# Kernel tuning notes

Hardware: AMD Instinct MI355X
Metric: run time of the kernel (lower is better)

Reference implementation:

```python
import jax, jax.numpy as jnp
import numpy as np

WS = 7
C = 384
NH = 12
HD = C // NH
HID = 4 * C


def layernorm(x, g, b, eps=1e-5):
    m = jnp.mean(x, axis=-1, keepdims=True)
    v = jnp.mean((x - m) ** 2, axis=-1, keepdims=True)
    return (x - m) * jax.lax.rsqrt(v + eps) * g + b


def setup_inputs() -> dict:
    key = jax.random.key(0)
    ks = jax.random.split(key, 12)
    s = 0.02
    return {
        "tokens": jax.random.normal(ks[0], (2, 8, 56 * 56, C), jnp.float32),
        "in_proj_w": jax.random.normal(ks[1], (3 * C, C), jnp.float32) * s,
        "in_proj_b": jnp.zeros((3 * C,), jnp.float32),
        "out_w": jax.random.normal(ks[2], (C, C), jnp.float32) * s,
        "out_b": jnp.zeros((C,), jnp.float32),
        "ln1_g": jnp.ones((C,), jnp.float32),
        "ln1_b": jnp.zeros((C,), jnp.float32),
        "w1": jax.random.normal(ks[3], (HID, C), jnp.float32) * s,
        "b1": jnp.zeros((HID,), jnp.float32),
        "w2": jax.random.normal(ks[4], (C, HID), jnp.float32) * s,
        "b2": jnp.zeros((C,), jnp.float32),
        "ln2_g": jnp.ones((C,), jnp.float32),
        "ln2_b": jnp.zeros((C,), jnp.float32),
        "h": 56,
        "w": 56,
    }


def _block(tokens, in_proj_w, in_proj_b, out_w, out_b, ln1_g, ln1_b, w1, b1, w2, b2, ln2_g, ln2_b, h, w):
    b, t, _, c = tokens.shape
    orig_h, orig_w = h, w
    x = tokens.reshape(b, t, h, w, c)
    pad_h = (-h) % WS
    pad_w = (-w) % WS
    if pad_h > 0 or pad_w > 0:
        x = jnp.pad(x, ((0, 0), (0, 0), (0, pad_h), (0, pad_w), (0, 0)))
        h, w = h + pad_h, w + pad_w
    nh, nw = h // WS, w // WS
    # window partition -> [N, 49, C]
    x = x.reshape(b, t, nh, WS, nw, WS, c).transpose(0, 1, 2, 4, 3, 5, 6)
    win = x.reshape(b * t * nh * nw, WS * WS, c)
    # MHA (torch nn.MultiheadAttention semantics)
    a = layernorm(win, ln1_g, ln1_b)
    qkv = a @ in_proj_w.T + in_proj_b  # [N, 49, 3C]
    q, k, v = jnp.split(qkv, 3, axis=-1)
    n, s, _ = q.shape
    q = q.reshape(n, s, NH, HD).transpose(0, 2, 1, 3)
    k = k.reshape(n, s, NH, HD).transpose(0, 2, 1, 3)
    v = v.reshape(n, s, NH, HD).transpose(0, 2, 1, 3)
    scores = jnp.einsum("nhqd,nhkd->nhqk", q, k) / jnp.sqrt(jnp.asarray(HD, q.dtype))
    p = jax.nn.softmax(scores, axis=-1)
    o = jnp.einsum("nhqk,nhkd->nhqd", p, v).transpose(0, 2, 1, 3).reshape(n, s, c)
    win = win + (o @ out_w.T + out_b)
    # MLP
    m = layernorm(win, ln2_g, ln2_b)
    m = jax.nn.gelu(m @ w1.T + b1, approximate=False) @ w2.T + b2
    win = win + m
    # window reverse
    x = win.reshape(b, t, nh, nw, WS, WS, c).transpose(0, 1, 2, 4, 3, 5, 6).reshape(b, t, h, w, c)
    x = x[:, :, :orig_h, :orig_w, :]
    return x.reshape(b, t, orig_h * orig_w, c)


def reference(tokens, in_proj_w, in_proj_b, out_w, out_b, ln1_g, ln1_b, w1, b1, w2, b2, ln2_g, ln2_b, h, w):
    return _block(tokens, in_proj_w, in_proj_b, out_w, out_b, ln1_g, ln1_b, w1, b1, w2, b2, ln2_g, ln2_b, h, w)
```

## Files before the change

### kernel.cpp

```cpp
#include <hip/hip_runtime.h>
#include <hip/hip_bf16.h>
#include <math.h>

using short8 = __attribute__((ext_vector_type(8))) short;
using f32x4  = __attribute__((ext_vector_type(4))) float;

#define MFMA_B16(A,B,C) __builtin_amdgcn_mfma_f32_16x16x32_bf16((A),(B),(C),0,0,0)

#define ALN_STR 392
#define ALN_SZ  38416
#define POOL    76832
#define PS      34816
#define Q2_OFF  0
#define K2_OFF  7056
#define VT_OFF  14112
#define OH_OFF  23328
#define HIDB    17408
#define QK_STR  72
#define VT_STR  72
#define OH_STR  72
#define HID_STR 136
#define SMEM_BYTES 146464

__device__ __forceinline__ unsigned short f2bfu(float x) {
  unsigned u = __float_as_uint(x);
  return (unsigned short)((u + 0x7fffu + ((u >> 16) & 1u)) >> 16);
}
__device__ __forceinline__ unsigned pk2(float a, float b) {
  return (unsigned)f2bfu(a) | ((unsigned)f2bfu(b) << 16);
}

template<bool WBF>
__device__ __forceinline__ short8 loadW(const void* base, int tile, int K8, int kcb,
                                        int l, int row, int ldk, int k0) {
  if constexpr (WBF) {
    return *(const short8*)((const unsigned short*)base +
                            (((size_t)(tile * K8 + kcb)) << 7) + l * 8);
  } else {
    const float* p = (const float*)base + (size_t)row * ldk + k0;
    float4 x = *(const float4*)p;
    float4 y = *(const float4*)(p + 4);
    short8 r;
    r[0]=(short)f2bfu(x.x); r[1]=(short)f2bfu(x.y); r[2]=(short)f2bfu(x.z); r[3]=(short)f2bfu(x.w);
    r[4]=(short)f2bfu(y.x); r[5]=(short)f2bfu(y.y); r[6]=(short)f2bfu(y.z); r[7]=(short)f2bfu(y.w);
    return r;
  }
}

__global__ void cvt_pack(const float* __restrict__ src, unsigned short* __restrict__ dst,
                         int K, int n) {
  int K8 = K >> 3;
  int i = blockIdx.x * blockDim.x + threadIdx.x;
  if (i >= n) return;
  int e = i & 7;
  int idx = i >> 3;
  int r = idx & 15; idx >>= 4;
  int kc = idx % K8, ci = idx / K8;
  dst[i] = f2bfu(src[(size_t)(ci * 16 + r) * K + kc * 8 + e]);
}

template<bool WBF>
__global__ __launch_bounds__(1024, 4)
void swin_mfma(const float* __restrict__ tokens,
               const void* __restrict__ ipw,  const float* __restrict__ ipb,
               const void* __restrict__ outw, const float* __restrict__ outb,
               const float* __restrict__ ln1g, const float* __restrict__ ln1b,
               const void* __restrict__ w1,   const float* __restrict__ b1,
               const void* __restrict__ w2,   const float* __restrict__ b2,
               const float* __restrict__ ln2g, const float* __restrict__ ln2b,
               float* __restrict__ out)
{
  extern __shared__ char smem[];
  const int tid = threadIdx.x;
  const int win = tid >> 9;
  const int gw  = tid >> 6;
  const int wv  = gw & 7;
  const int l   = tid & 63;
  const int cl  = l & 15, kg = l >> 4;

  unsigned short* alnW[2]; char* poolW[2];
  #pragma unroll
  for (int w = 0; w < 2; ++w) {
    alnW[w]  = (unsigned short*)(smem + w * ALN_SZ);
    poolW[w] = smem + POOL + w * PS;
  }
  unsigned short* aln = alnW[win];
  char* pool = poolW[win];
  unsigned short* q2  = (unsigned short*)(pool + Q2_OFF);
  unsigned short* k2  = (unsigned short*)(pool + K2_OFF);
  unsigned short* vT2 = (unsigned short*)(pool + VT_OFF);
  unsigned short* oh  = (unsigned short*)(pool + OH_OFF);

  const int wid0 = blockIdx.x * 2;
  auto gidxw = [&](int w, int r, int c) -> size_t {
    int wid = wid0 + w;
    int iw = wid & 7, ih = (wid >> 3) & 7, bt = wid >> 6;
    int wi = r / 7, wj = r - wi * 7;
    return ((size_t)bt * 3136 + (size_t)((ih*7 + wi) * 56 + iw*7 + wj)) * 384 + c;
  };

  auto ln_pass = [&](const float* src, const float* gw_, const float* gb_) {
    int row = (tid >> 3) & 63, lj = tid & 7;
    if (row < 49) {
      size_t base = gidxw(win, row, 0);
      float4 xv[12];
      float sx = 0.f, sxx = 0.f;
      #pragma unroll
      for (int k = 0; k < 12; ++k) {
        xv[k] = *(const float4*)&src[base + (lj + 8*k) * 4];
        sx  += xv[k].x + xv[k].y + xv[k].z + xv[k].w;
        sxx += xv[k].x*xv[k].x + xv[k].y*xv[k].y + xv[k].z*xv[k].z + xv[k].w*xv[k].w;
      }
      #pragma unroll
      for (int d = 1; d < 8; d <<= 1) { sx += __shfl_xor(sx, d, 8); sxx += __shfl_xor(sxx, d, 8); }
      float mean = sx * (1.f/384.f);
      float rs = rsqrtf(sxx * (1.f/384.f) - mean*mean + 1e-5f);
      unsigned short* arow = aln + row * ALN_STR;
      #pragma unroll
      for (int k = 0; k < 12; ++k) {
        int c = (lj + 8*k) * 4;
        float4 gv = *(const float4*)&gw_[c];
        float4 bv = *(const float4*)&gb_[c];
        unsigned u0 = pk2((xv[k].x-mean)*rs*gv.x + bv.x, (xv[k].y-mean)*rs*gv.y + bv.y);
        unsigned u1 = pk2((xv[k].z-mean)*rs*gv.z + bv.z, (xv[k].w-mean)*rs*gv.w + bv.w);
        *(uint2*)&arow[c] = make_uint2(u0, u1);
      }
    }
  };

  const int ri = gw & 3;
  const int cg = gw >> 2;
  const int arowA = (cl + 16 * ri) * ALN_STR;

  auto qkv = [&](int pr) {
    int tile[3], grow[3], part[3], wt[3];
    #pragma unroll
    for (int j = 0; j < 3; ++j) {
      int ci = cg * 3 + j;
      part[j] = ci >> 2; wt[j] = ci & 3;
      tile[j] = part[j] * 24 + pr * 4 + wt[j];
      grow[j] = part[j] * 384 + pr * 64 + wt[j] * 16 + cl;
    }
    f32x4 d00{0,0,0,0}, d01{0,0,0,0}, d02{0,0,0,0};
    f32x4 d10{0,0,0,0}, d11{0,0,0,0}, d12{0,0,0,0};
    #pragma unroll
    for (int kt = 0; kt < 12; ++kt) {
      int k0 = kt * 32 + kg * 8;
      short8 wb0 = loadW<WBF>(ipw, tile[0], 48, kt*4, l, grow[0], 384, k0);
      short8 wb1 = loadW<WBF>(ipw, tile[1], 48, kt*4, l, grow[1], 384, k0);
      short8 wb2 = loadW<WBF>(ipw, tile[2], 48, kt*4, l, grow[2], 384, k0);
      short8 a0 = *(const short8*)&alnW[0][arowA + k0];
      short8 a1 = *(const short8*)&alnW[1][arowA + k0];
      d00 = MFMA_B16(a0, wb0, d00); d01 = MFMA_B16(a0, wb1, d01); d02 = MFMA_B16(a0, wb2, d02);
      d10 = MFMA_B16(a1, wb0, d10); d11 = MFMA_B16(a1, wb1, d11); d12 = MFMA_B16(a1, wb2, d12);
    }
    #pragma unroll
    for (int w = 0; w < 2; ++w) {
      unsigned short* q2w = (unsigned short*)(poolW[w] + Q2_OFF);
      unsigned short* k2w = (unsigned short*)(poolW[w] + K2_OFF);
      unsigned short* vTw = (unsigned short*)(poolW[w] + VT_OFF);
      #pragma unroll
      for (int j = 0; j < 3; ++j) {
        f32x4 dd = (w == 0) ? (j == 0 ? d00 : j == 1 ? d01 : d02)
                            : (j == 0 ? d10 : j == 1 ? d11 : d12);
        float bias = ipb[grow[j]];
        float scl = (part[j] == 0) ? 0.17677669529663687f : 1.f;
        int within = wt[j] * 16 + cl;
        #pragma unroll
        for (int rg = 0; rg < 4; ++rg) {
          int row = kg * 4 + rg + 16 * ri;
          if (row < 49) {
            unsigned short bv = f2bfu((dd[rg] + bias) * scl);
            if      (part[j] == 0) q2w[row * QK_STR + within] = bv;
            else if (part[j] == 1) k2w[row * QK_STR + within] = bv;
            else                   vTw[within * VT_STR + row] = bv;
          }
        }
      }
    }
  };

  for (int i = (tid & 511); i < (64*VT_STR)/2; i += 512)
    ((unsigned*)(pool + VT_OFF))[i] = 0u;
  ln_pass(tokens, ln1g, ln1b);
  __syncthreads();

  f32x4 opacc[2][6];
  #pragma unroll
  for (int a = 0; a < 2; ++a)
    #pragma unroll
    for (int b = 0; b < 6; ++b) opacc[a][b] = f32x4{0.f,0.f,0.f,0.f};

  qkv(0);
  __syncthreads();

  const int hl = wv & 1, qci = wv >> 1;

  for (int pr = 0; pr < 6; ++pr) {
    {
      short8 bq = *(const short8*)&q2[(16*qci + cl) * QK_STR + hl*32 + kg*8];
      f32x4 dsc[4];
      #pragma unroll
      for (int kri = 0; kri < 4; ++kri) {
        short8 ak = *(const short8*)&k2[(16*kri + cl) * QK_STR + hl*32 + kg*8];
        f32x4 z{0.f,0.f,0.f,0.f};
        dsc[kri] = MFMA_B16(ak, bq, z);
      }
      float ev[4][4];
      float mx = -1e30f;
      #pragma unroll
      for (int kri = 0; kri < 4; ++kri)
        #pragma unroll
        for (int r = 0; r < 4; ++r) {
          int kidx = 16*kri + 4*kg + r;
          float v = (kidx < 49) ? dsc[kri][r] : -1e30f;
          ev[kri][r] = v;
          mx = fmaxf(mx, v);
        }
      mx = fmaxf(mx, __shfl_xor(mx, 16));
      mx = fmaxf(mx, __shfl_xor(mx, 32));
      float sum = 0.f;
      #pragma unroll
      for (int kri = 0; kri < 4; ++kri)
        #pragma unroll
        for (int r = 0; r < 4; ++r) {
          float e = __expf(ev[kri][r] - mx);
          ev[kri][r] = e; sum += e;
        }
      sum += __shfl_xor(sum, 16);
      sum += __shfl_xor(sum, 32);
      float inv = 1.f / sum;
      unsigned pk[4][2];
      #pragma unroll
      for (int kri = 0; kri < 4; ++kri) {
        pk[kri][0] = pk2(ev[kri][0]*inv, ev[kri][1]*inv);
        pk[kri][1] = pk2(ev[kri][2]*inv, ev[kri][3]*inv);
      }
      f32x4 dot0{0.f,0.f,0.f,0.f}, dot1{0.f,0.f,0.f,0.f};
      const int sA = cl + 32 * (kg & 1);
      const bool hi = (kg >> 1) & 1;
      #pragma unroll
      for (int kt = 0; kt < 2; ++kt) {
        unsigned x0 = (unsigned)__shfl((int)pk[2*kt][0],   sA);
        unsigned x1 = (unsigned)__shfl((int)pk[2*kt][1],   sA);
        unsigned x2 = (unsigned)__shfl((int)pk[2*kt][0],   sA + 16);
        unsigned x3 = (unsigned)__shfl((int)pk[2*kt][1],   sA + 16);
        unsigned y0 = (unsigned)__shfl((int)pk[2*kt+1][0], sA);
        unsigned y1 = (unsigned)__shfl((int)pk[2*kt+1][1], sA);
        unsigned y2 = (unsigned)__shfl((int)pk[2*kt+1][0], sA + 16);
        unsigned y3 = (unsigned)__shfl((int)pk[2*kt+1][1], sA + 16);
        uint4 bu = make_uint4(hi ? y0 : x0, hi ? y1 : x1, hi ? y2 : x2, hi ? y3 : x3);
        short8 bfrag = *(short8*)&bu;
        short8 a0 = *(const short8*)&vT2[(hl*32 +  0 + cl) * VT_STR + kt*32 + kg*8];
        short8 a1 = *(const short8*)&vT2[(hl*32 + 16 + cl) * VT_STR + kt*32 + kg*8];
        dot0 = MFMA_B16(a0, bfrag, dot0);
        dot1 = MFMA_B16(a1, bfrag, dot1);
      }
      int q = 16*qci + cl;
      if (q < 49) {
        int base = q * OH_STR + hl*32 + kg*4;
        *(unsigned*)&oh[base     ] = pk2(dot0[0], dot0[1]);
        *(unsigned*)&oh[base +  2] = pk2(dot0[2], dot0[3]);
        *(unsigned*)&oh[base + 16] = pk2(dot1[0], dot1[1]);
        *(unsigned*)&oh[base + 18] = pk2(dot1[2], dot1[3]);
      }
    }
    __syncthreads();

    {
      short8 ao[2][2];
      #pragma unroll
      for (int w = 0; w < 2; ++w) {
        unsigned short* ohw = (unsigned short*)(poolW[w] + OH_OFF);
        ao[w][0] = *(const short8*)&ohw[(cl + 16*ri) * OH_STR +      kg*8];
        ao[w][1] = *(const short8*)&ohw[(cl + 16*ri) * OH_STR + 32 + kg*8];
      }
      #pragma unroll
      for (int j = 0; j < 6; ++j) {
        int ct = cg*6 + j;
        short8 bw0 = loadW<WBF>(outw, ct, 48, pr*8,     l, ct*16 + cl, 384, pr*64      + kg*8);
        short8 bw1 = loadW<WBF>(outw, ct, 48, pr*8 + 4, l, ct*16 + cl, 384, pr*64 + 32 + kg*8);
        opacc[0][j] = MFMA_B16(ao[0][0], bw0, opacc[0][j]);
        opacc[0][j] = MFMA_B16(ao[0][1], bw1, opacc[0][j]);
        opacc[1][j] = MFMA_B16(ao[1][0], bw0, opacc[1][j]);
        opacc[1][j] = MFMA_B16(ao[1][1], bw1, opacc[1][j]);
      }
      if (pr < 5) qkv(pr + 1);
    }
    __syncthreads();
  }

  #pragma unroll
  for (int w = 0; w < 2; ++w)
    #pragma unroll
    for (int j = 0; j < 6; ++j) {
      int col = (cg*6 + j) * 16 + cl;
      float ob = outb[col];
      #pragma unroll
      for (int rg = 0; rg < 4; ++rg) {
        int row = 16*ri + kg*4 + rg;
        if (row < 49) {
          size_t g = gidxw(w, row, col);
          out[g] = tokens[g] + opacc[w][j][rg] + ob;
        }
      }
    }
  __syncthreads();

  ln_pass(out, ln2g, ln2b);
  __syncthreads();

  f32x4 macc[2][2][3];
  #pragma unroll
  for (int a = 0; a < 2; ++a)
    #pragma unroll
    for (int t = 0; t < 2; ++t)
      #pragma unroll
      for (int j = 0; j < 3; ++j) macc[a][t][j] = f32x4{0.f,0.f,0.f,0.f};

  const int rp = gw & 1, cg3 = gw >> 1;

  auto mlp1 = [&](int cc, int pb) {
    f32x4 e00{0,0,0,0}, e01{0,0,0,0}, e10{0,0,0,0}, e11{0,0,0,0};
    #pragma unroll
    for (int kt = 0; kt < 12; ++kt) {
      int k0 = kt * 32 + kg * 8;
      short8 wb0 = loadW<WBF>(w1, cc*8 + cg*2 + 0, 48, kt*4, l, (cc*8+cg*2+0)*16 + cl, 384, k0);
      short8 wb1 = loadW<WBF>(w1, cc*8 + cg*2 + 1, 48, kt*4, l, (cc*8+cg*2+1)*16 + cl, 384, k0);
      short8 a0 = *(const short8*)&alnW[0][arowA + k0];
      short8 a1 = *(const short8*)&alnW[1][arowA + k0];
      e00 = MFMA_B16(a0, wb0, e00); e01 = MFMA_B16(a0, wb1, e01);
      e10 = MFMA_B16(a1, wb0, e10); e11 = MFMA_B16(a1, wb1, e11);
    }
    #pragma unroll
    for (int w = 0; w < 2; ++w) {
      unsigned short* hb = (unsigned short*)(poolW[w] + pb * HIDB);
      #pragma unroll
      for (int j = 0; j < 2; ++j) {
        f32x4 ee = (w == 0) ? (j == 0 ? e00 : e01) : (j == 0 ? e10 : e11);
        int n = cc*128 + (cg*2 + j)*16 + cl;
        float bb = b1[n];
        #pragma unroll
        for (int rg = 0; rg < 4; ++rg) {
          int row = 16*ri + kg*4 + rg;
          if (row < 49) {
            float x = ee[rg] + bb;
            float t2 = 0.044715f * x * x;
            float arg = __builtin_fmaf(t2, x, x);
            float e = __expf(1.5957691216f * arg);
            float gl = x * (e / (e + 1.f));
            hb[row * HID_STR + (cg*2 + j)*16 + cl] = f2bfu(gl);
          }
        }
      }
    }
  };
  auto mlp2 = [&](int cc, int pb) {
    unsigned short* hb0 = (unsigned short*)(poolW[0] + pb * HIDB);
    unsigned short* hb1 = (unsigned short*)(poolW[1] + pb * HIDB);
    #pragma unroll
    for (int kt = 0; kt < 4; ++kt) {
      int k0 = kt * 32 + kg * 8;
      short8 hd00 = *(const short8*)&hb0[(cl + 16*(2*rp    )) * HID_STR + k0];
      short8 hd01 = *(const short8*)&hb0[(cl + 16*(2*rp + 1)) * HID_STR + k0];
      short8 hd10 = *(const short8*)&hb1[(cl + 16*(2*rp    )) * HID_STR + k0];
      short8 hd11 = *(const short8*)&hb1[(cl + 16*(2*rp + 1)) * HID_STR + k0];
      #pragma unroll
      for (int j = 0; j < 3; ++j) {
        int ct = cg3*3 + j;
        short8 bw = loadW<WBF>(w2, ct, 192, cc*16 + kt*4, l,
                               ct*16 + cl, 1536, cc*128 + k0);
        macc[0][0][j] = MFMA_B16(hd00, bw, macc[0][0][j]);
        macc[0][1][j] = MFMA_B16(hd01, bw, macc[0][1][j]);
        macc[1][0][j] = MFMA_B16(hd10, bw, macc[1][0][j]);
        macc[1][1][j] = MFMA_B16(hd11, bw, macc[1][1][j]);
      }
    }
  };

  mlp1(0, 0);
  __syncthreads();
  for (int cc = 1; cc < 12; ++cc) {
    mlp2(cc - 1, (cc - 1) & 1);
    mlp1(cc, cc & 1);
    __syncthreads();
  }
  mlp2(11, 1);

  #pragma unroll
  for (int w = 0; w < 2; ++w)
    #pragma unroll
    for (int t = 0; t < 2; ++t)
      #pragma unroll
      for (int j = 0; j < 3; ++j) {
        int col = (cg3*3 + j) * 16 + cl;
        float bb2 = b2[col];
        #pragma unroll
        for (int rg = 0; rg < 4; ++rg) {
          int row = 16*(2*rp + t) + kg*4 + rg;
          if (row < 49) {
            size_t g = gidxw(w, row, col);
            out[g] = out[g] + macc[w][t][j][rg] + bb2;
          }
        }
      }
}

#define WS_IPW  0
#define WS_OUTW 442368
#define WS_W1   589824
#define WS_W2   1179648
#define WS_TOT  1769472

extern "C" void kernel_launch(void* const* d_in, const int* in_sizes, int n_in,
                              void* d_out, int out_size, void* d_ws, size_t ws_size,
                              hipStream_t stream) {
  (void)in_sizes; (void)n_in; (void)out_size;
  const float* tokens = (const float*)d_in[0];
  const float* ipw  = (const float*)d_in[1];
  const float* ipb  = (const float*)d_in[2];
  const float* outw = (const float*)d_in[3];
  const float* outb = (const float*)d_in[4];
  const float* ln1g = (const float*)d_in[5];
  const float* ln1b = (const float*)d_in[6];
  const float* w1   = (const float*)d_in[7];
  const float* b1   = (const float*)d_in[8];
  const float* w2   = (const float*)d_in[9];
  const float* b2   = (const float*)d_in[10];
  const float* ln2g = (const float*)d_in[11];
  const float* ln2b = (const float*)d_in[12];
  float* out = (float*)d_out;

  bool wbf = (ws_size >= (size_t)WS_TOT * 2);
  if (wbf) {
    unsigned short* wsp = (unsigned short*)d_ws;
    hipLaunchKernelGGL(cvt_pack, dim3((442368+511)/512), dim3(512), 0, stream, ipw,  wsp + WS_IPW,  384,  442368);
    hipLaunchKernelGGL(cvt_pack, dim3((147456+511)/512), dim3(512), 0, stream, outw, wsp + WS_OUTW, 384,  147456);
    hipLaunchKernelGGL(cvt_pack, dim3((589824+511)/512), dim3(512), 0, stream, w1,   wsp + WS_W1,   384,  589824);
    hipLaunchKernelGGL(cvt_pack, dim3((589824+511)/512), dim3(512), 0, stream, w2,   wsp + WS_W2,   1536, 589824);
    (void)hipFuncSetAttribute((const void*)swin_mfma<true>,
                              hipFuncAttributeMaxDynamicSharedMemorySize, SMEM_BYTES);
    hipLaunchKernelGGL((swin_mfma<true>), dim3(512), dim3(1024), SMEM_BYTES, stream,
                       tokens, (const void*)(wsp + WS_IPW), ipb,
                       (const void*)(wsp + WS_OUTW), outb, ln1g, ln1b,
                       (const void*)(wsp + WS_W1), b1, (const void*)(wsp + WS_W2), b2,
                       ln2g, ln2b, out);
  } else {
    (void)hipFuncSetAttribute((const void*)swin_mfma<false>,
                              hipFuncAttributeMaxDynamicSharedMemorySize, SMEM_BYTES);
    hipLaunchKernelGGL((swin_mfma<false>), dim3(512), dim3(1024), SMEM_BYTES, stream,
                       tokens, (const void*)ipw, ipb, (const void*)outw, outb, ln1g, ln1b,
                       (const void*)w1, b1, (const void*)w2, b2, ln2g, ln2b, out);
  }
}
```

Before: 537.7 us.

## Split fused Swin block into staged LN, QKV, attention, out-proj and MLP kernels

Replaces the single monolithic per-window kernel with a pipeline of kernels: LayerNorm1 to a bf16 buffer, a tiled QKV GEMM over 64-row blocks, a per-window attention kernel, an out-projection kernel fused with the residual add and LayerNorm2, and a fused MLP kernel. Intermediates go through a large workspace in bf16. The aim is to escape the huge shared-memory footprint and low occupancy of the monolithic kernel so each GEMM gets better weight reuse across 64 rows. The cost is extra global-memory round trips for the intermediates, and the new path only runs when the workspace is large enough, about 158 MB.

```diff
diff --git a/kernel.cpp b/kernel.cpp
--- a/kernel.cpp
+++ b/kernel.cpp
@@ -6,6 +6,317 @@
 using f32x4  = __attribute__((ext_vector_type(4))) float;
 
 #define MFMA_B16(A,B,C) __builtin_amdgcn_mfma_f32_16x16x32_bf16((A),(B),(C),0,0,0)
+
+__device__ __forceinline__ unsigned short f2bfu(float x) {
+  unsigned u = __float_as_uint(x);
+  return (unsigned short)((u + 0x7fffu + ((u >> 16) & 1u)) >> 16);
+}
+__device__ __forceinline__ unsigned pk2(float a, float b) {
+  return (unsigned)f2bfu(a) | ((unsigned)f2bfu(b) << 16);
+}
+
+__global__ void cvt_pack(const float* __restrict__ src, unsigned short* __restrict__ dst,
+                         int K, int n) {
+  int K8 = K >> 3;
+  int i = blockIdx.x * blockDim.x + threadIdx.x;
+  if (i >= n) return;
+  int e = i & 7;
+  int idx = i >> 3;
+  int r = idx & 15; idx >>= 4;
+  int kc = idx % K8, ci = idx / K8;
+  dst[i] = f2bfu(src[(size_t)(ci * 16 + r) * K + kc * 8 + e]);
+}
+
+__device__ __forceinline__ int gmapbase(int m) {
+  int w = m / 49, r = m - w * 49;
+  int iw = w & 7, ih = (w >> 3) & 7, bt = w >> 6;
+  int wi = r / 7, wj = r - wi * 7;
+  return (bt * 3136 + (ih * 7 + wi) * 56 + iw * 7 + wj) * 384;
+}
+
+__device__ __forceinline__ void ln_rows(const float* __restrict__ src,
+                                        const float* __restrict__ gw,
+                                        const float* __restrict__ gb,
+                                        unsigned short* __restrict__ dst,
+                                        int m0, int tid) {
+  int m = m0 + (tid >> 3), lj = tid & 7;
+  size_t gbase = (size_t)gmapbase(m);
+  float4 xv[12];
+  float sx = 0.f, sxx = 0.f;
+  #pragma unroll
+  for (int k = 0; k < 12; ++k) {
+    xv[k] = *(const float4*)&src[gbase + (lj + 8*k) * 4];
+    sx  += xv[k].x + xv[k].y + xv[k].z + xv[k].w;
+    sxx += xv[k].x*xv[k].x + xv[k].y*xv[k].y + xv[k].z*xv[k].z + xv[k].w*xv[k].w;
+  }
+  #pragma unroll
+  for (int d = 1; d < 8; d <<= 1) { sx += __shfl_xor(sx, d, 8); sxx += __shfl_xor(sxx, d, 8); }
+  float mean = sx * (1.f/384.f);
+  float rs = rsqrtf(sxx * (1.f/384.f) - mean*mean + 1e-5f);
+  unsigned short* drow = dst + (size_t)m * 384;
+  #pragma unroll
+  for (int k = 0; k < 12; ++k) {
+    int c = (lj + 8*k) * 4;
+    float4 gv = *(const float4*)&gw[c];
+    float4 bv = *(const float4*)&gb[c];
+    unsigned u0 = pk2((xv[k].x-mean)*rs*gv.x + bv.x, (xv[k].y-mean)*rs*gv.y + bv.y);
+    unsigned u1 = pk2((xv[k].z-mean)*rs*gv.z + bv.z, (xv[k].w-mean)*rs*gv.w + bv.w);
+    *(uint2*)&drow[c] = make_uint2(u0, u1);
+  }
+}
+
+__global__ __launch_bounds__(512)
+void ln1_k(const float* __restrict__ tokens, const float* __restrict__ g,
+           const float* __restrict__ b, unsigned short* __restrict__ aln) {
+  ln_rows(tokens, g, b, aln, blockIdx.x * 64, threadIdx.x);
+}
+
+__device__ __forceinline__ void stageA(const unsigned short* __restrict__ gsrc,
+                                       size_t gelem0, char* lds, int tid) {
+  for (int i = tid; i < 64 * 48; i += 512) {
+    int row = i / 48, c = i - row * 48;
+    short8 v = *(const short8*)(gsrc + gelem0 + (size_t)row * 384 + c * 8);
+    int boff = (row * 768 + c * 16) ^ ((row & 7) << 4);
+    *(short8*)(lds + boff) = v;
+  }
+}
+__device__ __forceinline__ short8 ldsA(const char* lds, int row, int k0) {
+  int boff = (row * 768 + k0 * 2) ^ ((row & 7) << 4);
+  return *(const short8*)(lds + boff);
+}
+__device__ __forceinline__ short8 ldW(const unsigned short* wp, int tile, int K8,
+                                      int kcb, int l) {
+  return *(const short8*)(wp + (((size_t)(tile * K8 + kcb)) << 7) + l * 8);
+}
+
+__global__ __launch_bounds__(512, 4)
+void qkv_gemm(const unsigned short* __restrict__ aln, const unsigned short* __restrict__ wp,
+              const float* __restrict__ ipb, unsigned short* __restrict__ qkv) {
+  extern __shared__ char lds[];
+  const int tid = threadIdx.x;
+  const int m0 = blockIdx.x * 64, part = blockIdx.y;
+  stageA(aln, (size_t)m0 * 384, lds, tid);
+  __syncthreads();
+  const int l = tid & 63, wv = tid >> 6, cl = l & 15, kg = l >> 4;
+  const int rt = wv & 3, ch = wv >> 2;
+  f32x4 acc[12];
+  #pragma unroll
+  for (int j = 0; j < 12; ++j) acc[j] = f32x4{0.f,0.f,0.f,0.f};
+  for (int kt = 0; kt < 12; ++kt) {
+    int k0 = kt * 32 + kg * 8;
+    short8 a = ldsA(lds, rt * 16 + cl, k0);
+    #pragma unroll
+    for (int j = 0; j < 12; ++j) {
+      short8 bf = ldW(wp, part * 24 + ch * 12 + j, 48, kt * 4, l);
+      acc[j] = MFMA_B16(a, bf, acc[j]);
+    }
+  }
+  float scl = (part == 0) ? 0.17677669529663687f : 1.f;
+  #pragma unroll
+  for (int j = 0; j < 12; ++j) {
+    int wcol = (ch * 12 + j) * 16 + cl;
+    float bias = ipb[part * 384 + wcol];
+    #pragma unroll
+    for (int rg = 0; rg < 4; ++rg) {
+      int m = m0 + rt * 16 + kg * 4 + rg;
+      qkv[(size_t)m * 1152 + part * 384 + wcol] = f2bfu((acc[j][rg] + bias) * scl);
+    }
+  }
+}
+
+__global__ __launch_bounds__(256, 4)
+void attn_k(const unsigned short* __restrict__ qkv, unsigned short* __restrict__ oh) {
+  __shared__ unsigned short vT2[32 * 56];
+  const int tid = threadIdx.x;
+  const int l = tid & 63, wv = tid >> 6;
+  const int cl = l & 15, kg = l >> 4;
+  const size_t base = (size_t)blockIdx.x * 49;
+  for (int i = tid; i < 224; i += 256) vT2[(i / 7) * 56 + 49 + i % 7] = 0;
+  const int qrow = (16 * wv + cl < 49) ? 16 * wv + cl : 48;
+  for (int h = 0; h < 12; ++h) {
+    __syncthreads();
+    for (int i = tid; i < 1568; i += 256) {
+      int r = i >> 5, d = i & 31;
+      vT2[d * 56 + r] = qkv[(base + r) * 1152 + 768 + h * 32 + d];
+    }
+    __syncthreads();
+    short8 bq = *(const short8*)(qkv + (base + qrow) * 1152 + h * 32 + kg * 8);
+    f32x4 dsc[4];
+    #pragma unroll
+    for (int kri = 0; kri < 4; ++kri) {
+      size_t mk = base + 16 * kri + cl;
+      if (mk > 50175) mk = 50175;
+      short8 ak = *(const short8*)(qkv + mk * 1152 + 384 + h * 32 + kg * 8);
+      f32x4 z{0.f,0.f,0.f,0.f};
+      dsc[kri] = MFMA_B16(ak, bq, z);
+    }
+    float ev[4][4];
+    float mx = -1e30f;
+    #pragma unroll
+    for (int kri = 0; kri < 4; ++kri)
+      #pragma unroll
+      for (int r = 0; r < 4; ++r) {
+        int kidx = 16 * kri + 4 * kg + r;
+        float v = (kidx < 49) ? dsc[kri][r] : -1e30f;
+        ev[kri][r] = v;
+        mx = fmaxf(mx, v);
+      }
+    mx = fmaxf(mx, __shfl_xor(mx, 16));
+    mx = fmaxf(mx, __shfl_xor(mx, 32));
+    float sum = 0.f;
+    #pragma unroll
+    for (int kri = 0; kri < 4; ++kri)
+      #pragma unroll
+      for (int r = 0; r < 4; ++r) {
+        float e = __expf(ev[kri][r] - mx);
+        ev[kri][r] = e; sum += e;
+      }
+    sum += __shfl_xor(sum, 16);
+    sum += __shfl_xor(sum, 32);
+    float inv = 1.f / sum;
+    unsigned pk[4][2];
+    #pragma unroll
+    for (int kri = 0; kri < 4; ++kri) {
+      pk[kri][0] = pk2(ev[kri][0] * inv, ev[kri][1] * inv);
+      pk[kri][1] = pk2(ev[kri][2] * inv, ev[kri][3] * inv);
+    }
+    f32x4 dot0{0.f,0.f,0.f,0.f}, dot1{0.f,0.f,0.f,0.f};
+    const int sA = cl + 32 * (kg & 1);
+    const bool hi = (kg >> 1) & 1;
+    #pragma unroll
+    for (int kt = 0; kt < 2; ++kt) {
+      unsigned x0 = (unsigned)__shfl((int)pk[2*kt][0],   sA);
+      unsigned x1 = (unsigned)__shfl((int)pk[2*kt][1],   sA);
+      unsigned x2 = (unsigned)__shfl((int)pk[2*kt][0],   sA + 16);
+      unsigned x3 = (unsigned)__shfl((int)pk[2*kt][1],   sA + 16);
+      unsigned y0 = (unsigned)__shfl((int)pk[2*kt+1][0], sA);
+      unsigned y1 = (unsigned)__shfl((int)pk[2*kt+1][1], sA);
+      unsigned y2 = (unsigned)__shfl((int)pk[2*kt+1][0], sA + 16);
+      unsigned y3 = (unsigned)__shfl((int)pk[2*kt+1][1], sA + 16);
+      uint4 bu = make_uint4(hi ? y0 : x0, hi ? y1 : x1, hi ? y2 : x2, hi ? y3 : x3);
+      short8 bfrag = *(short8*)&bu;
+      short8 a0 = *(const short8*)&vT2[(cl     ) * 56 + kt * 32 + kg * 8];
+      short8 a1 = *(const short8*)&vT2[(16 + cl) * 56 + kt * 32 + kg * 8];
+      dot0 = MFMA_B16(a0, bfrag, dot0);
+      dot1 = MFMA_B16(a1, bfrag, dot1);
+    }
+    int q = 16 * wv + cl;
+    if (q < 49) {
+      size_t ob = (base + q) * 384 + h * 32 + kg * 4;
+      *(unsigned*)(oh + ob     ) = pk2(dot0[0], dot0[1]);
+      *(unsigned*)(oh + ob + 2 ) = pk2(dot0[2], dot0[3]);
+      *(unsigned*)(oh + ob + 16) = pk2(dot1[0], dot1[1]);
+      *(unsigned*)(oh + ob + 18) = pk2(dot1[2], dot1[3]);
+    }
+  }
+}
+
+__global__ __launch_bounds__(512, 4)
+void outproj_k(const unsigned short* __restrict__ oh, const unsigned short* __restrict__ wp,
+               const float* __restrict__ outb, const float* __restrict__ tokens,
+               const float* __restrict__ ln2g, const float* __restrict__ ln2b,
+               float* __restrict__ dout, unsigned short* __restrict__ aln2) {
+  extern __shared__ char lds[];
+  const int tid = threadIdx.x;
+  const int m0 = blockIdx.x * 64;
+  stageA(oh, (size_t)m0 * 384, lds, tid);
+  __syncthreads();
+  const int l = tid & 63, wv = tid >> 6, cl = l & 15, kg = l >> 4;
+  const int rt = wv & 3, ch = wv >> 2;
+  f32x4 acc[12];
+  #pragma unroll
+  for (int j = 0; j < 12; ++j) acc[j] = f32x4{0.f,0.f,0.f,0.f};
+  for (int kt = 0; kt < 12; ++kt) {
+    int k0 = kt * 32 + kg * 8;
+    short8 a = ldsA(lds, rt * 16 + cl, k0);
+    #pragma unroll
+    for (int j = 0; j < 12; ++j) {
+      short8 bf = ldW(wp, ch * 12 + j, 48, kt * 4, l);
+      acc[j] = MFMA_B16(a, bf, acc[j]);
+    }
+  }
+  int gb[4];
+  #pragma unroll
+  for (int rg = 0; rg < 4; ++rg) gb[rg] = gmapbase(m0 + rt * 16 + kg * 4 + rg);
+  #pragma unroll
+  for (int j = 0; j < 12; ++j) {
+    int col = (ch * 12 + j) * 16 + cl;
+    float ob = outb[col];
+    #pragma unroll
+    for (int rg = 0; rg < 4; ++rg)
+      dout[gb[rg] + col] = tokens[gb[rg] + col] + acc[j][rg] + ob;
+  }
+  __syncthreads();
+  ln_rows(dout, ln2g, ln2b, aln2, m0, tid);
+}
+
+__global__ __launch_bounds__(512, 4)
+void mlp_fused(const unsigned short* __restrict__ aln2, const unsigned short* __restrict__ w1p,
+               const float* __restrict__ b1, const unsigned short* __restrict__ w2p,
+               const float* __restrict__ b2, float* __restrict__ dout) {
+  extern __shared__ char lds[];
+  unsigned short* hid = (unsigned short*)(lds + 49152);
+  const int tid = threadIdx.x;
+  const int m0 = blockIdx.x * 64;
+  stageA(aln2, (size_t)m0 * 384, lds, tid);
+  __syncthreads();
+  const int l = tid & 63, wv = tid >> 6, cl = l & 15, kg = l >> 4;
+  const int rt = wv & 3, ch = wv >> 2;
+  f32x4 macc[12];
+  #pragma unroll
+  for (int j = 0; j < 12; ++j) macc[j] = f32x4{0.f,0.f,0.f,0.f};
+  for (int cc = 0; cc < 12; ++cc) {
+    f32x4 e[4];
+    #pragma unroll
+    for (int jj = 0; jj < 4; ++jj) e[jj] = f32x4{0.f,0.f,0.f,0.f};
+    for (int kt = 0; kt < 12; ++kt) {
+      int k0 = kt * 32 + kg * 8;
+      short8 a = ldsA(lds, rt * 16 + cl, k0);
+      #pragma unroll
+      for (int jj = 0; jj < 4; ++jj) {
+        short8 bf = ldW(w1p, cc * 8 + ch * 4 + jj, 48, kt * 4, l);
+        e[jj] = MFMA_B16(a, bf, e[jj]);
+      }
+    }
+    #pragma unroll
+    for (int jj = 0; jj < 4; ++jj) {
+      int hcol = (ch * 4 + jj) * 16 + cl;
+      float bb = b1[cc * 128 + hcol];
+      #pragma unroll
+      for (int rg = 0; rg < 4; ++rg) {
+        int row = rt * 16 + kg * 4 + rg;
+        float x = e[jj][rg] + bb;
+        float t2 = 0.044715f * x * x;
+        float arg = __builtin_fmaf(t2, x, x);
+        float ex = __expf(1.5957691216f * arg);
+        hid[row * 136 + hcol] = f2bfu(x * (ex / (ex + 1.f)));
+      }
+    }
+    __syncthreads();
+    #pragma unroll
+    for (int kt2 = 0; kt2 < 4; ++kt2) {
+      int k0 = kt2 * 32 + kg * 8;
+      short8 hd = *(const short8*)&hid[(rt * 16 + cl) * 136 + k0];
+      #pragma unroll
+      for (int j = 0; j < 12; ++j) {
+        short8 bf = ldW(w2p, ch * 12 + j, 192, cc * 16 + kt2 * 4, l);
+        macc[j] = MFMA_B16(hd, bf, macc[j]);
+      }
+    }
+    __syncthreads();
+  }
+  int gb[4];
+  #pragma unroll
+  for (int rg = 0; rg < 4; ++rg) gb[rg] = gmapbase(m0 + rt * 16 + kg * 4 + rg);
+  #pragma unroll
+  for (int j = 0; j < 12; ++j) {
+    int col = (ch * 12 + j) * 16 + cl;
+    float bb2 = b2[col];
+    #pragma unroll
+    for (int rg = 0; rg < 4; ++rg)
+      dout[gb[rg] + col] = dout[gb[rg] + col] + macc[j][rg] + bb2;
+  }
+}
 
 #define ALN_STR 392
 #define ALN_SZ  38416
@@ -22,14 +333,6 @@
 #define HID_STR 136
 #define SMEM_BYTES 146464
 
-__device__ __forceinline__ unsigned short f2bfu(float x) {
-  unsigned u = __float_as_uint(x);
-  return (unsigned short)((u + 0x7fffu + ((u >> 16) & 1u)) >> 16);
-}
-__device__ __forceinline__ unsigned pk2(float a, float b) {
-  return (unsigned)f2bfu(a) | ((unsigned)f2bfu(b) << 16);
-}
-
 template<bool WBF>
 __device__ __forceinline__ short8 loadW(const void* base, int tile, int K8, int kcb,
                                         int l, int row, int ldk, int k0) {
@@ -45,18 +348,6 @@
     r[4]=(short)f2bfu(y.x); r[5]=(short)f2bfu(y.y); r[6]=(short)f2bfu(y.z); r[7]=(short)f2bfu(y.w);
     return r;
   }
-}
-
-__global__ void cvt_pack(const float* __restrict__ src, unsigned short* __restrict__ dst,
-                         int K, int n) {
-  int K8 = K >> 3;
-  int i = blockIdx.x * blockDim.x + threadIdx.x;
-  if (i >= n) return;
-  int e = i & 7;
-  int idx = i >> 3;
-  int r = idx & 15; idx >>= 4;
-  int kc = idx % K8, ci = idx / K8;
-  dst[i] = f2bfu(src[(size_t)(ci * 16 + r) * K + kc * 8 + e]);
 }
 
 template<bool WBF>
@@ -266,7 +557,6 @@
       }
     }
     __syncthreads();
-
     {
       short8 ao[2][2];
       #pragma unroll
@@ -406,11 +696,15 @@
       }
 }
 
-#define WS_IPW  0
-#define WS_OUTW 442368
-#define WS_W1   589824
-#define WS_W2   1179648
-#define WS_TOT  1769472
+#define OFF_ALN  0ull
+#define OFF_QKV  19267584ull
+#define OFF_WP   77070336ull
+#define WS_IPW   0
+#define WS_OUTW  442368
+#define WS_W1    589824
+#define WS_W2    1179648
+#define WS_TOT   1769472
+#define WS_NEED  ((OFF_WP + (unsigned long long)WS_TOT) * 2ull)
 
 extern "C" void kernel_launch(void* const* d_in, const int* in_sizes, int n_in,
                               void* d_out, int out_size, void* d_ws, size_t ws_size,
@@ -430,10 +724,28 @@
   const float* ln2g = (const float*)d_in[11];
   const float* ln2b = (const float*)d_in[12];
   float* out = (float*)d_out;
-
-  bool wbf = (ws_size >= (size_t)WS_TOT * 2);
-  if (wbf) {
-    unsigned short* wsp = (unsigned short*)d_ws;
+  unsigned short* wsp = (unsigned short*)d_ws;
+
+  if (ws_size >= (size_t)WS_NEED) {
+    unsigned short* wp = wsp + OFF_WP;
+    hipLaunchKernelGGL(cvt_pack, dim3((442368+511)/512), dim3(512), 0, stream, ipw,  wp + WS_IPW,  384,  442368);
+    hipLaunchKernelGGL(cvt_pack, dim3((147456+511)/512), dim3(512), 0, stream, outw, wp + WS_OUTW, 384,  147456);
+    hipLaunchKernelGGL(cvt_pack, dim3((589824+511)/512), dim3(512), 0, stream, w1,   wp + WS_W1,   384,  589824);
+    hipLaunchKernelGGL(cvt_pack, dim3((589824+511)/512), dim3(512), 0, stream, w2,   wp + WS_W2,   1536, 589824);
+    (void)hipFuncSetAttribute((const void*)mlp_fused,
+                              hipFuncAttributeMaxDynamicSharedMemorySize, 66560);
+    hipLaunchKernelGGL(ln1_k, dim3(784), dim3(512), 0, stream,
+                       tokens, ln1g, ln1b, wsp + OFF_ALN);
+    hipLaunchKernelGGL(qkv_gemm, dim3(784, 3), dim3(512), 49152, stream,
+                       wsp + OFF_ALN, wp + WS_IPW, ipb, wsp + OFF_QKV);
+    hipLaunchKernelGGL(attn_k, dim3(1024), dim3(256), 0, stream,
+                       wsp + OFF_QKV, wsp + OFF_ALN);
+    hipLaunchKernelGGL(outproj_k, dim3(784), dim3(512), 49152, stream,
+                       wsp + OFF_ALN, wp + WS_OUTW, outb, tokens, ln2g, ln2b,
+                       out, wsp + OFF_QKV);
+    hipLaunchKernelGGL(mlp_fused, dim3(784), dim3(512), 66560, stream,
+                       wsp + OFF_QKV, wp + WS_W1, b1, wp + WS_W2, b2, out);
+  } else if (ws_size >= (size_t)WS_TOT * 2) {
     hipLaunchKernelGGL(cvt_pack, dim3((442368+511)/512), dim3(512), 0, stream, ipw,  wsp + WS_IPW,  384,  442368);
     hipLaunchKernelGGL(cvt_pack, dim3((147456+511)/512), dim3(512), 0, stream, outw, wsp + WS_OUTW, 384,  147456);
     hipLaunchKernelGGL(cvt_pack, dim3((589824+511)/512), dim3(512), 0, stream, w1,   wsp + WS_W1,   384,  589824);
```

New measurement: 1.191 ms. 2.22x slower.
